# Kernel tuning notes

Hardware: AMD Instinct MI355X
Metric: run time of the kernel (lower is better)

Reference implementation:

```python
import jax, jax.numpy as jnp
import numpy as np

B, T, S, D, H, E, K, FF = 4, 1024, 1024, 1024, 16, 8, 2, 4096
DH = D // H
EPS = 1e-5

def layernorm(x, g, b):
    m = x.mean(-1, keepdims=True)
    v = x.var(-1, keepdims=True)
    return (x - m) / jnp.sqrt(v + EPS) * g + b

def mha(q, k, v, mask, wq, bq, wk, bk, wv, bv, wo, bo):
    Bq, Tq, _ = q.shape
    Tk = k.shape[1]
    Q = (q @ wq + bq).reshape(Bq, Tq, H, DH).transpose(0, 2, 1, 3)
    Kh = (k @ wk + bk).reshape(Bq, Tk, H, DH).transpose(0, 2, 1, 3)
    V = (v @ wv + bv).reshape(Bq, Tk, H, DH).transpose(0, 2, 1, 3)
    scores = jnp.einsum('bhqd,bhkd->bhqk', Q, Kh) / (DH ** 0.5)
    scores = jnp.where(mask != 0, scores, jnp.float32(-1e9))
    A = jax.nn.softmax(scores, axis=-1)
    O = jnp.einsum('bhqk,bhkd->bhqd', A, V).transpose(0, 2, 1, 3).reshape(Bq, Tq, D)
    return O @ wo + bo

def sparse_moe(x, wg, bg, w1, b1, w2, b2):
    # x: [B,T,D] -> tokens [N,D]
    Bx, Tx, _ = x.shape
    xt = x.reshape(-1, D)
    N = xt.shape[0]
    probs = jax.nn.softmax(xt @ wg + bg, axis=-1)          # [N,E]
    topv, topi = jax.lax.top_k(probs, K)                    # [N,K]
    topv = topv / topv.sum(-1, keepdims=True)
    gates = jnp.zeros((N, E), xt.dtype).at[jnp.arange(N)[:, None], topi].set(topv)
    h = jax.nn.relu(jnp.einsum('nd,edh->enh', xt, w1) + b1[:, None, :])  # [E,N,FF]
    y = jnp.einsum('enh,ehd->end', h, w2) + b2[:, None, :]               # [E,N,D]
    out = jnp.einsum('ne,end->nd', gates, y)
    return out.reshape(Bx, Tx, D)

def setup_inputs() -> dict:
    key = jax.random.key(0)
    ks = jax.random.split(key, 32)
    r = lambda k, s: jax.random.normal(k, s, dtype=jnp.float32) * 0.02
    inp = {
        'x': jax.random.normal(ks[0], (B, T, D), jnp.float32),
        'encoder_out': jax.random.normal(ks[1], (B, S, D), jnp.float32),
        'src_attn_mask': jnp.ones((B, 1, 1, S), jnp.int32),
        'tgt_attn_mask': jnp.tril(jnp.ones((T, T), jnp.int32))[None, None],
        'ln1_g': jnp.ones((D,), jnp.float32), 'ln1_b': jnp.zeros((D,), jnp.float32),
        'ln2_g': jnp.ones((D,), jnp.float32), 'ln2_b': jnp.zeros((D,), jnp.float32),
        'ln3_g': jnp.ones((D,), jnp.float32), 'ln3_b': jnp.zeros((D,), jnp.float32),
        'wq1': r(ks[2], (D, D)), 'bq1': jnp.zeros((D,), jnp.float32),
        'wk1': r(ks[3], (D, D)), 'bk1': jnp.zeros((D,), jnp.float32),
        'wv1': r(ks[4], (D, D)), 'bv1': jnp.zeros((D,), jnp.float32),
        'wo1': r(ks[5], (D, D)), 'bo1': jnp.zeros((D,), jnp.float32),
        'wq2': r(ks[6], (D, D)), 'bq2': jnp.zeros((D,), jnp.float32),
        'wk2': r(ks[7], (D, D)), 'bk2': jnp.zeros((D,), jnp.float32),
        'wv2': r(ks[8], (D, D)), 'bv2': jnp.zeros((D,), jnp.float32),
        'wo2': r(ks[9], (D, D)), 'bo2': jnp.zeros((D,), jnp.float32),
        'wg': r(ks[10], (D, E)), 'bg': jnp.zeros((E,), jnp.float32),
        'w1': r(ks[11], (E, D, FF)), 'b1': jnp.zeros((E, FF), jnp.float32),
        'w2': r(ks[12], (E, FF, D)), 'b2': jnp.zeros((E, D), jnp.float32),
    }
    return inp

def reference(x, encoder_out, src_attn_mask, tgt_attn_mask,
              ln1_g, ln1_b, ln2_g, ln2_b, ln3_g, ln3_b,
              wq1, bq1, wk1, bk1, wv1, bv1, wo1, bo1,
              wq2, bq2, wk2, bk2, wv2, bv2, wo2, bo2,
              wg, bg, w1, b1, w2, b2):
    # pre-norm residual: x + sublayer(LN(x)); dropout=0 (eval)
    n1 = layernorm(x, ln1_g, ln1_b)
    h1 = x + mha(n1, n1, n1, tgt_attn_mask, wq1, bq1, wk1, bk1, wv1, bv1, wo1, bo1)
    n2 = layernorm(h1, ln2_g, ln2_b)
    h2 = h1 + mha(n2, encoder_out, encoder_out, src_attn_mask, wq2, bq2, wk2, bk2, wv2, bv2, wo2, bo2)
    n3 = layernorm(h2, ln3_g, ln3_b)
    h3 = h2 + sparse_moe(n3, wg, bg, w1, b1, w2, b2)
    return h3
```

## Files before the change

### kernel.cpp

```cpp
#include <hip/hip_runtime.h>

typedef unsigned short u16;
typedef float f32x4 __attribute__((ext_vector_type(4)));
typedef short s16x8 __attribute__((ext_vector_type(8)));
typedef u16   u16x4 __attribute__((ext_vector_type(4)));

#define DEV static __device__ __forceinline__

DEV u16 f2b(float f){
  unsigned u = __builtin_bit_cast(unsigned, f);
  u += 0x7fffu + ((u >> 16) & 1u);
  return (u16)(u >> 16);
}
DEV float b2f(u16 h){ unsigned u = ((unsigned)h) << 16; return __builtin_bit_cast(float, u); }
DEV void tsplit(float v, u16& hv, u16& lv){
  unsigned u = __builtin_bit_cast(unsigned, v);
  hv = (u16)(u >> 16);
  float rest = v - __builtin_bit_cast(float, u & 0xffff0000u);
  lv = (u16)(__builtin_bit_cast(unsigned, rest) >> 16);
}
DEV float fexp2(float x){ float r; asm("v_exp_f32 %0, %1" : "=v"(r) : "v"(x)); return r; }

DEV void glds16(const u16* g, u16* l){
  __builtin_amdgcn_global_load_lds(
      (const __attribute__((address_space(1))) void*)g,
      (__attribute__((address_space(3))) void*)l, 16, 0, 0);
}

DEV f32x4 mfma3(s16x8 ah, s16x8 al, s16x8 bh, s16x8 bl, f32x4 c){
  c = __builtin_amdgcn_mfma_f32_16x16x32_bf16(ah, bh, c, 0, 0, 0);
  c = __builtin_amdgcn_mfma_f32_16x16x32_bf16(ah, bl, c, 0, 0, 0);
  c = __builtin_amdgcn_mfma_f32_16x16x32_bf16(al, bh, c, 0, 0, 0);
  return c;
}

constexpr int TT = 1024, DM = 1024, NE = 8, FFD = 4096;
constexpr int NTOK = 4096;

struct Ptr8 { const float* p[8]; };

__global__ __launch_bounds__(256) void trans8_k(Ptr8 srcs, u16* __restrict__ dh, u16* __restrict__ dl){
  __shared__ float tl[64][65];
  const float* src = srcs.p[blockIdx.z];
  u16* dsth = dh + (size_t)blockIdx.z * 1024 * 1024;
  u16* dstl = dl + (size_t)blockIdx.z * 1024 * 1024;
  const int tid = threadIdx.x;
  const int r0 = blockIdx.y * 64, c0 = blockIdx.x * 64;
  const int ty = tid >> 4, tx = tid & 15;
#pragma unroll
  for (int i = 0; i < 4; i++){
    int row = ty + i * 16;
    f32x4 v = *(const f32x4*)&src[(size_t)(r0 + row) * 1024 + c0 + tx * 4];
#pragma unroll
    for (int j = 0; j < 4; j++) tl[row][tx * 4 + j] = v[j];
  }
  __syncthreads();
#pragma unroll
  for (int i = 0; i < 4; i++){
    int drow = ty + i * 16;
    u16x4 oh, ol;
#pragma unroll
    for (int j = 0; j < 4; j++){
      float v = tl[tx * 4 + j][drow];
      u16 hh, ll; tsplit(v, hh, ll);
      oh[j] = hh; ol[j] = ll;
    }
    *(u16x4*)&dsth[(size_t)(c0 + drow) * 1024 + r0 + tx * 4] = oh;
    *(u16x4*)&dstl[(size_t)(c0 + drow) * 1024 + r0 + tx * 4] = ol;
  }
}

__global__ __launch_bounds__(256) void transb_k(const float* __restrict__ src0, u16* __restrict__ dst0, int R, int C){
  __shared__ float tl[64][65];
  const float* src = src0 + (size_t)blockIdx.z * R * C;
  u16* dst = dst0 + (size_t)blockIdx.z * R * C;
  const int tid = threadIdx.x;
  const int r0 = blockIdx.y * 64, c0 = blockIdx.x * 64;
  const int ty = tid >> 4, tx = tid & 15;
#pragma unroll
  for (int i = 0; i < 4; i++){
    int row = ty + i * 16;
    f32x4 v = *(const f32x4*)&src[(size_t)(r0 + row) * C + c0 + tx * 4];
#pragma unroll
    for (int j = 0; j < 4; j++) tl[row][tx * 4 + j] = v[j];
  }
  __syncthreads();
#pragma unroll
  for (int i = 0; i < 4; i++){
    int drow = ty + i * 16;
    u16x4 o;
#pragma unroll
    for (int j = 0; j < 4; j++) o[j] = f2b(tl[tx * 4 + j][drow]);
    *(u16x4*)&dst[(size_t)(c0 + drow) * R + r0 + tx * 4] = o;
  }
}

__global__ __launch_bounds__(256) void split_k(const float* __restrict__ src,
                                               u16* __restrict__ dh, u16* __restrict__ dl, int n4){
  int i = blockIdx.x * 256 + threadIdx.x;
  if (i < n4){
    f32x4 v = *(const f32x4*)&src[(size_t)i * 4];
    u16x4 oh, ol;
#pragma unroll
    for (int j = 0; j < 4; j++){ u16 hh, ll; tsplit(v[j], hh, ll); oh[j] = hh; ol[j] = ll; }
    *(u16x4*)&dh[(size_t)i * 4] = oh;
    *(u16x4*)&dl[(size_t)i * 4] = ol;
  }
}

__global__ __launch_bounds__(256) void ln_k(const float* __restrict__ x, const float* __restrict__ g,
                                            const float* __restrict__ b,
                                            u16* __restrict__ outH, u16* __restrict__ outL){
  __shared__ float red[8];
  const int row = blockIdx.x, tid = threadIdx.x, l = tid & 63, wave = tid >> 6;
  f32x4 v = *(const f32x4*)&x[(size_t)row * DM + tid * 4];
  float s = v[0] + v[1] + v[2] + v[3];
  float sq = v[0]*v[0] + v[1]*v[1] + v[2]*v[2] + v[3]*v[3];
#pragma unroll
  for (int m = 1; m < 64; m <<= 1){ s += __shfl_xor(s, m); sq += __shfl_xor(sq, m); }
  if (l == 0){ red[wave] = s; red[4 + wave] = sq; }
  __syncthreads();
  float tot = red[0] + red[1] + red[2] + red[3];
  float totq = red[4] + red[5] + red[6] + red[7];
  float mean = tot * (1.0f / DM);
  float var = totq * (1.0f / DM) - mean * mean;
  float rstd = rsqrtf(var + 1e-5f);
  f32x4 gg = *(const f32x4*)&g[tid * 4];
  f32x4 bb = *(const f32x4*)&b[tid * 4];
  u16x4 oh, ol;
#pragma unroll
  for (int j = 0; j < 4; j++){
    float y = (v[j] - mean) * rstd * gg[j] + bb[j];
    u16 hh, ll; tsplit(y, hh, ll); oh[j] = hh; ol[j] = ll;
  }
  *(u16x4*)&outH[(size_t)row * DM + tid * 4] = oh;
  if (outL) *(u16x4*)&outL[(size_t)row * DM + tid * 4] = ol;
}

struct QKVArgs {
  const u16* ah[3]; const u16* al[3]; const float* bias[3];
};

__global__ __launch_bounds__(256) void gemm_qkv3_k(
    QKVArgs args, const u16* __restrict__ Bhp, const u16* __restrict__ Blp,
    u16* __restrict__ QH, u16* __restrict__ QL,
    u16* __restrict__ KH, u16* __restrict__ KL,
    u16* __restrict__ VTH, u16* __restrict__ VTL)
{
  constexpr int K = DM;
  __shared__ alignas(16) u16 LAh[128 * 32], LAl[128 * 32];
  __shared__ alignas(16) u16 LBh[128 * 32], LBl[128 * 32];
  const int tid = threadIdx.x, l = tid & 63, wave = tid >> 6;
  const int seg = blockIdx.z;
  const int m0 = blockIdx.y * 128, n0 = blockIdx.x * 128;
  const int r0 = tid >> 2, seg8 = (tid & 3) * 8;
  const u16* gAh = args.ah[seg] + (size_t)(m0 + r0) * K + seg8;
  const u16* gAl = args.al[seg] + (size_t)(m0 + r0) * K + seg8;
  const u16* gBh = Bhp + (size_t)(seg * 1024 + n0 + r0) * K + seg8;
  const u16* gBl = Blp + (size_t)(seg * 1024 + n0 + r0) * K + seg8;
  u16* wAh = &LAh[wave * 512]; u16* wAl = &LAl[wave * 512];
  u16* wBh = &LBh[wave * 512]; u16* wBl = &LBl[wave * 512];
  const size_t K64 = (size_t)64 * K;
  f32x4 acc[4][4];
#pragma unroll
  for (int i = 0; i < 4; i++)
#pragma unroll
    for (int j = 0; j < 4; j++) acc[i][j] = f32x4{0.f, 0.f, 0.f, 0.f};
  const int wm = (wave >> 1) * 64, wn = (wave & 1) * 64;
  for (int kt = 0; kt < K; kt += 32){
    __syncthreads();
    glds16(gAh + kt, wAh); glds16(gAh + kt + K64, wAh + 2048);
    glds16(gAl + kt, wAl); glds16(gAl + kt + K64, wAl + 2048);
    glds16(gBh + kt, wBh); glds16(gBh + kt + K64, wBh + 2048);
    glds16(gBl + kt, wBl); glds16(gBl + kt + K64, wBl + 2048);
    __syncthreads();
    s16x8 afh[4], afl[4], bfh[4], bfl[4];
#pragma unroll
    for (int i = 0; i < 4; i++){
      int ar = (wm + i * 16 + (l & 15)) * 32 + (l >> 4) * 8;
      int br = (wn + i * 16 + (l & 15)) * 32 + (l >> 4) * 8;
      afh[i] = *(const s16x8*)&LAh[ar];
      afl[i] = *(const s16x8*)&LAl[ar];
      bfh[i] = *(const s16x8*)&LBh[br];
      bfl[i] = *(const s16x8*)&LBl[br];
    }
#pragma unroll
    for (int i = 0; i < 4; i++)
#pragma unroll
      for (int j = 0; j < 4; j++)
        acc[i][j] = mfma3(afh[i], afl[i], bfh[j], bfl[j], acc[i][j]);
  }
  const float* bp = args.bias[seg];
  u16* DH = (seg == 0) ? QH : KH;
  u16* DL = (seg == 0) ? QL : KL;
#pragma unroll
  for (int i = 0; i < 4; i++)
#pragma unroll
    for (int r = 0; r < 4; r++){
      int row = m0 + wm + i * 16 + (l >> 4) * 4 + r;
#pragma unroll
      for (int j = 0; j < 4; j++){
        int col = n0 + wn + j * 16 + (l & 15);
        float v = acc[i][j][r] + bp[col];
        u16 hv, lv; tsplit(v, hv, lv);
        if (seg == 2){
          int bb = row >> 10, tq = row & 1023, hh = col >> 6, dd = col & 63;
          size_t vi = ((size_t)((bb << 4) + hh) * 64 + dd) * 1024 + tq;
          VTH[vi] = hv; VTL[vi] = lv;
        } else {
          size_t idx = (size_t)row * 1024 + col;
          DH[idx] = hv; DL[idx] = lv;
        }
      }
    }
}

__global__ __launch_bounds__(256) void gemm_o64_k(
    const u16* __restrict__ Ahp, const u16* __restrict__ Alp,
    const u16* __restrict__ Bhp, const u16* __restrict__ Blp,
    const float* __restrict__ bias, const float* __restrict__ res,
    float* __restrict__ Cf)
{
  constexpr int K = DM;
  __shared__ alignas(16) u16 LAh[64 * 32], LAl[64 * 32];
  __shared__ alignas(16) u16 LBh[128 * 32], LBl[128 * 32];
  const int tid = threadIdx.x, l = tid & 63, wave = tid >> 6;
  const int m0 = blockIdx.y * 64, n0 = blockIdx.x * 128;
  const int rA = tid >> 2, seg8 = (tid & 3) * 8;
  const u16* gAh = Ahp + (size_t)(m0 + rA) * K + seg8;
  const u16* gAl = Alp + (size_t)(m0 + rA) * K + seg8;
  const u16* gBh = Bhp + (size_t)(n0 + rA) * K + seg8;
  const u16* gBl = Blp + (size_t)(n0 + rA) * K + seg8;
  u16* wAh = &LAh[wave * 512]; u16* wAl = &LAl[wave * 512];
  u16* wBh = &LBh[wave * 512]; u16* wBl = &LBl[wave * 512];
  const size_t K64 = (size_t)64 * K;
  f32x4 acc[2][4];
#pragma unroll
  for (int i = 0; i < 2; i++)
#pragma unroll
    for (int j = 0; j < 4; j++) acc[i][j] = f32x4{0.f, 0.f, 0.f, 0.f};
  const int wm = (wave >> 1) * 32, wn = (wave & 1) * 64;
  for (int kt = 0; kt < K; kt += 32){
    __syncthreads();
    glds16(gAh + kt, wAh);
    glds16(gAl + kt, wAl);
    glds16(gBh + kt, wBh); glds16(gBh + kt + K64, wBh + 2048);
    glds16(gBl + kt, wBl); glds16(gBl + kt + K64, wBl + 2048);
    __syncthreads();
    s16x8 afh[2], afl[2], bfh[4], bfl[4];
#pragma unroll
    for (int i = 0; i < 2; i++){
      int ar = (wm + i * 16 + (l & 15)) * 32 + (l >> 4) * 8;
      afh[i] = *(const s16x8*)&LAh[ar];
      afl[i] = *(const s16x8*)&LAl[ar];
    }
#pragma unroll
    for (int j = 0; j < 4; j++){
      int br = (wn + j * 16 + (l & 15)) * 32 + (l >> 4) * 8;
      bfh[j] = *(const s16x8*)&LBh[br];
      bfl[j] = *(const s16x8*)&LBl[br];
    }
#pragma unroll
    for (int i = 0; i < 2; i++)
#pragma unroll
      for (int j = 0; j < 4; j++)
        acc[i][j] = mfma3(afh[i], afl[i], bfh[j], bfl[j], acc[i][j]);
  }
#pragma unroll
  for (int i = 0; i < 2; i++)
#pragma unroll
    for (int r = 0; r < 4; r++){
      int row = m0 + wm + i * 16 + (l >> 4) * 4 + r;
#pragma unroll
      for (int j = 0; j < 4; j++){
        int col = n0 + wn + j * 16 + (l & 15);
        size_t idx = (size_t)row * 1024 + col;
        Cf[idx] = acc[i][j][r] + bias[col] + res[idx];
      }
    }
}

template<bool CAUSAL>
__global__ __launch_bounds__(512) void attn5_k(
    const u16* __restrict__ Qh, const u16* __restrict__ Ql,
    const u16* __restrict__ Kh, const u16* __restrict__ Kl,
    const u16* __restrict__ Vth, const u16* __restrict__ Vtl,
    const int* __restrict__ mask,
    float* __restrict__ OP0, float* __restrict__ OP1,
    float* __restrict__ LS0, float* __restrict__ LS1,
    int Tq, int Tk)
{
  constexpr float CS = 0.125f * 1.4426950408889634f;
  __shared__ alignas(16) u16 KhiL[2048], KloL[2048];
  __shared__ alignas(16) u16 VhiL[2048], VloL[2048];
  __shared__ alignas(16) u16 Plh[8][640], Pll[8][640];
  const int tid = threadIdx.x, l = tid & 63, wave = tid >> 6;
  const int id = blockIdx.x;
  const int bh = ((id >> 3) & 7) * 8 + (id & 7);
  const int b = bh >> 4, h = bh & 15;
  const int qt = (id >> 6) & 7, ks = id >> 9;
  const int q0 = qt * 128;
  float* __restrict__ OP = ks ? OP1 : OP0;
  float* __restrict__ LS = ks ? LS1 : LS0;
  const int ktBeg = ks * 512;
  int lim = CAUSAL ? (q0 + 128) : Tk;
  if (lim > Tk) lim = Tk;
  int ktEnd = (ks + 1) * 512;
  if (ktEnd > lim) ktEnd = lim;

  const int qr = q0 + wave * 16 + (l & 15);
  s16x8 qah[2], qal[2];
#pragma unroll
  for (int kb = 0; kb < 2; kb++){
    size_t base = (size_t)(b * Tq + qr) * DM + h * 64 + kb * 32 + (l >> 4) * 8;
    qah[kb] = *(const s16x8*)(Qh + base);
    qal[kb] = *(const s16x8*)(Ql + base);
  }

  const int sHalf = wave >> 2;
  const int sw = wave & 3;
  const int iS = sw * 64 + l;
  const int keyS = iS >> 3, cKS = iS & 7;
  const u16* gK = (sHalf ? Kl : Kh)
      + (size_t)(b * Tk + ktBeg + keyS) * DM + h * 64 + ((cKS ^ (keyS & 7)) * 8);
  u16* dK = (sHalf ? KloL : KhiL) + sw * 512;
  const int dS = iS >> 2, cVS = iS & 3;
  const size_t vgbase = (size_t)bh * 64 * 1024;
  const u16* gV = (sHalf ? Vtl : Vth)
      + vgbase + (size_t)dS * 1024 + ktBeg + ((cVS ^ ((dS >> 1) & 3)) * 8);
  u16* dV = (sHalf ? VloL : VhiL) + sw * 512;

  float lsum[4] = {0.f, 0.f, 0.f, 0.f};
  f32x4 oacc[4];
#pragma unroll
  for (int nb = 0; nb < 4; nb++) oacc[nb] = f32x4{0.f, 0.f, 0.f, 0.f};
  const int qgr = q0 + wave * 16 + (l >> 4) * 4;

  for (int kt = ktBeg; kt < ktEnd; kt += 32){
    __syncthreads();
    glds16(gK, dK); gK += (size_t)32 * DM;
    glds16(gV, dV); gV += 32;
    __syncthreads();

    f32x4 s[2];
#pragma unroll
    for (int n = 0; n < 2; n++){
      s[n] = f32x4{0.f, 0.f, 0.f, 0.f};
      const int key = n * 16 + (l & 15);
      const int sK = (key & 7);
#pragma unroll
      for (int kb = 0; kb < 2; kb++){
        const int cK = kb * 4 + (l >> 4);
        const int off = key * 64 + ((cK ^ sK) * 8);
        s16x8 kh = *(const s16x8*)&KhiL[off];
        s16x8 klo = *(const s16x8*)&KloL[off];
        s[n] = __builtin_amdgcn_mfma_f32_16x16x32_bf16(qah[kb], kh, s[n], 0, 0, 0);
        s[n] = __builtin_amdgcn_mfma_f32_16x16x32_bf16(qah[kb], klo, s[n], 0, 0, 0);
        s[n] = __builtin_amdgcn_mfma_f32_16x16x32_bf16(qal[kb], kh, s[n], 0, 0, 0);
      }
    }
    int key0 = kt + (l & 15), key1 = key0 + 16;
    int mv0 = 1, mv1 = 1;
    if (!CAUSAL && mask){ mv0 = mask[b * Tk + key0]; mv1 = mask[b * Tk + key1]; }
#pragma unroll
    for (int r = 0; r < 4; r++){
      float p0, p1;
      if (CAUSAL){
        int qg = qgr + r;
        p0 = (key0 <= qg) ? fexp2(s[0][r] * CS) : 0.f;
        p1 = (key1 <= qg) ? fexp2(s[1][r] * CS) : 0.f;
      } else {
        p0 = mv0 ? fexp2(s[0][r] * CS) : 0.f;
        p1 = mv1 ? fexp2(s[1][r] * CS) : 0.f;
      }
      lsum[r] += p0 + p1;
      int po = ((l >> 4) * 4 + r) * 40 + (l & 15);
      u16 h0, l0, h1, l1;
      tsplit(p0, h0, l0); tsplit(p1, h1, l1);
      Plh[wave][po] = h0;      Pll[wave][po] = l0;
      Plh[wave][po + 16] = h1; Pll[wave][po + 16] = l1;
    }
    s16x8 pah = *(const s16x8*)&Plh[wave][(l & 15) * 40 + (l >> 4) * 8];
    s16x8 pal = *(const s16x8*)&Pll[wave][(l & 15) * 40 + (l >> 4) * 8];
#pragma unroll
    for (int nb = 0; nb < 4; nb++){
      const int d = nb * 16 + (l & 15);
      const int off = d * 32 + (((l >> 4) ^ ((d >> 1) & 3)) * 8);
      s16x8 vfh = *(const s16x8*)&VhiL[off];
      s16x8 vfl = *(const s16x8*)&VloL[off];
      oacc[nb] = mfma3(pah, pal, vfh, vfl, oacc[nb]);
    }
  }
#pragma unroll
  for (int r = 0; r < 4; r++){
    float s = lsum[r];
    s += __shfl_xor(s, 1); s += __shfl_xor(s, 2);
    s += __shfl_xor(s, 4); s += __shfl_xor(s, 8);
    int qg = qgr + r;
    if ((l & 15) == 0) LS[(size_t)bh * 1024 + qg] = s;
#pragma unroll
    for (int nb = 0; nb < 4; nb++)
      OP[(size_t)(b * Tq + qg) * DM + h * 64 + nb * 16 + (l & 15)] = oacc[nb][r];
  }
}

__global__ __launch_bounds__(256) void norm_k(
    const float* __restrict__ OP0, const float* __restrict__ OP1,
    const float* __restrict__ LS0, const float* __restrict__ LS1,
    u16* __restrict__ Oh, u16* __restrict__ Ol)
{
  const int t = blockIdx.x, c = threadIdx.x * 4;
  const int b = t >> 10, q = t & 1023, h = c >> 6;
  const size_t li = (size_t)(b * 16 + h) * 1024 + q;
  float inv = 1.0f / (LS0[li] + LS1[li]);
  f32x4 o0 = *(const f32x4*)&OP0[(size_t)t * DM + c];
  f32x4 o1 = *(const f32x4*)&OP1[(size_t)t * DM + c];
  u16x4 oh, ol;
#pragma unroll
  for (int j = 0; j < 4; j++){
    float v = (o0[j] + o1[j]) * inv;
    u16 hh, ll; tsplit(v, hh, ll); oh[j] = hh; ol[j] = ll;
  }
  *(u16x4*)&Oh[(size_t)t * DM + c] = oh;
  *(u16x4*)&Ol[(size_t)t * DM + c] = ol;
}

__global__ __launch_bounds__(256) void moe_gate_k(const float* __restrict__ X,
    const float* __restrict__ g3, const float* __restrict__ b3,
    const float* __restrict__ wg, const float* __restrict__ bg,
    int* __restrict__ cnt, int* __restrict__ perm,
    int* __restrict__ toke, int* __restrict__ tokp, float* __restrict__ tokg)
{
  const int wave = threadIdx.x >> 6, l = threadIdx.x & 63;
  const int t = blockIdx.x * 4 + wave;
  float xv[16];
  float s = 0.f, sq = 0.f;
#pragma unroll
  for (int i = 0; i < 16; i++){
    xv[i] = X[(size_t)t * DM + l + i * 64];
    s += xv[i]; sq += xv[i] * xv[i];
  }
#pragma unroll
  for (int m = 1; m < 64; m <<= 1){ s += __shfl_xor(s, m); sq += __shfl_xor(sq, m); }
  float mean = s * (1.0f / DM);
  float var = sq * (1.0f / DM) - mean * mean;
  float rstd = rsqrtf(var + 1e-5f);
  float acc[8];
#pragma unroll
  for (int e = 0; e < 8; e++) acc[e] = 0.f;
#pragma unroll
  for (int i = 0; i < 16; i++){
    int k = l + i * 64;
    float xn = (xv[i] - mean) * rstd * g3[k] + b3[k];
    f32x4 wa = *(const f32x4*)&wg[k * 8];
    f32x4 wb = *(const f32x4*)&wg[k * 8 + 4];
#pragma unroll
    for (int j = 0; j < 4; j++){ acc[j] += xn * wa[j]; acc[4 + j] += xn * wb[j]; }
  }
#pragma unroll
  for (int e = 0; e < 8; e++)
#pragma unroll
    for (int m = 1; m < 64; m <<= 1) acc[e] += __shfl_xor(acc[e], m);
  if (l == 0){
    float lg[8];
#pragma unroll
    for (int e = 0; e < 8; e++) lg[e] = acc[e] + bg[e];
    float mx = lg[0];
#pragma unroll
    for (int e = 1; e < 8; e++) mx = fmaxf(mx, lg[e]);
    float ex[8]; float sum = 0.f;
#pragma unroll
    for (int e = 0; e < 8; e++){ ex[e] = expf(lg[e] - mx); sum += ex[e]; }
    int i0 = 0;
    for (int e = 1; e < 8; e++) if (ex[e] > ex[i0]) i0 = e;
    int i1 = (i0 == 0) ? 1 : 0;
    for (int e = 0; e < 8; e++) if (e != i0 && ex[e] > ex[i1]) i1 = e;
    float p0 = ex[i0] / sum, p1 = ex[i1] / sum;
    float gs = p0 + p1;
    int pos0 = atomicAdd(&cnt[i0], 1);
    int pos1 = atomicAdd(&cnt[i1], 1);
    perm[i0 * 4096 + pos0] = t;
    perm[i1 * 4096 + pos1] = t;
    toke[2 * t] = i0; toke[2 * t + 1] = i1;
    tokp[2 * t] = pos0; tokp[2 * t + 1] = pos1;
    tokg[2 * t] = p0 / gs; tokg[2 * t + 1] = p1 / gs;
  }
}

__global__ void offsets_k(const int* __restrict__ cnt, int* __restrict__ off){
  if (threadIdx.x == 0){
    int a = 0;
    for (int e = 0; e < 8; e++){ off[e] = a; a += cnt[e]; }
  }
}

__global__ __launch_bounds__(256) void gemm_moe1_k(
    const u16* __restrict__ X, const u16* __restrict__ W1t, const float* __restrict__ b1,
    const int* __restrict__ perm, const int* __restrict__ cnt, const int* __restrict__ off,
    u16* __restrict__ Hb)
{
  const int e = blockIdx.z;
  const int Ce = cnt[e];
  const int mt = blockIdx.y;
  if (mt * 128 >= Ce) return;
  __shared__ alignas(16) u16 Asl[128 * 32];
  __shared__ alignas(16) u16 Bsl[128 * 32];
  const int tid = threadIdx.x, l = tid & 63, wave = tid >> 6;
  const int n0 = blockIdx.x * 128;
  const int r0 = tid >> 2, seg = (tid & 3) * 8;
  const int rl0 = mt * 128 + r0, rl1 = rl0 + 64;
  const int g0 = perm[e * 4096 + (rl0 < Ce ? rl0 : Ce - 1)];
  const int g1 = perm[e * 4096 + (rl1 < Ce ? rl1 : Ce - 1)];
  const u16* gA0 = X + (size_t)g0 * DM + seg;
  const u16* gA1 = X + (size_t)g1 * DM + seg;
  const u16* gB = W1t + (size_t)e * FFD * DM + (size_t)(n0 + r0) * DM + seg;
  u16* wA = &Asl[wave * 512]; u16* wB = &Bsl[wave * 512];
  f32x4 acc[4][4];
#pragma unroll
  for (int i = 0; i < 4; i++)
#pragma unroll
    for (int j = 0; j < 4; j++) acc[i][j] = f32x4{0.f,0.f,0.f,0.f};
  const int wm = (wave >> 1) * 64, wn = (wave & 1) * 64;
  for (int kt = 0; kt < DM; kt += 32){
    __syncthreads();
    glds16(gA0 + kt, wA); glds16(gA1 + kt, wA + 2048);
    glds16(gB + kt, wB);  glds16(gB + kt + (size_t)64 * DM, wB + 2048);
    __syncthreads();
    s16x8 af[4], bfr[4];
#pragma unroll
    for (int i = 0; i < 4; i++){
      af[i]  = *(const s16x8*)&Asl[(wm + i * 16 + (l & 15)) * 32 + (l >> 4) * 8];
      bfr[i] = *(const s16x8*)&Bsl[(wn + i * 16 + (l & 15)) * 32 + (l >> 4) * 8];
    }
#pragma unroll
    for (int i = 0; i < 4; i++)
#pragma unroll
      for (int j = 0; j < 4; j++)
        acc[i][j] = __builtin_amdgcn_mfma_f32_16x16x32_bf16(af[i], bfr[j], acc[i][j], 0, 0, 0);
  }
  const int base = off[e];
#pragma unroll
  for (int i = 0; i < 4; i++)
#pragma unroll
    for (int r = 0; r < 4; r++){
      int rloc = mt * 128 + wm + i * 16 + (l >> 4) * 4 + r;
      if (rloc < Ce){
#pragma unroll
        for (int j = 0; j < 4; j++){
          int col = n0 + wn + j * 16 + (l & 15);
          float v = acc[i][j][r] + b1[e * FFD + col];
          v = fmaxf(v, 0.f);
          Hb[(size_t)(base + rloc) * FFD + col] = f2b(v);
        }
      }
    }
}

__global__ __launch_bounds__(256) void gemm_moe2_k(
    const u16* __restrict__ Hb, const u16* __restrict__ W2t,
    const int* __restrict__ cnt, const int* __restrict__ off, float* __restrict__ Y)
{
  const int e = blockIdx.z;
  const int Ce = cnt[e];
  const int mt = blockIdx.y;
  if (mt * 128 >= Ce) return;
  __shared__ alignas(16) u16 Asl[128 * 32];
  __shared__ alignas(16) u16 Bsl[128 * 32];
  const int tid = threadIdx.x, l = tid & 63, wave = tid >> 6;
  const int n0 = blockIdx.x * 128;
  const int r0 = tid >> 2, seg = (tid & 3) * 8;
  const int base = off[e];
  const int rl0 = mt * 128 + r0, rl1 = rl0 + 64;
  const int a0r = base + (rl0 < Ce ? rl0 : Ce - 1);
  const int a1r = base + (rl1 < Ce ? rl1 : Ce - 1);
  const u16* gA0 = Hb + (size_t)a0r * FFD + seg;
  const u16* gA1 = Hb + (size_t)a1r * FFD + seg;
  const u16* gB = W2t + (size_t)e * DM * FFD + (size_t)(n0 + r0) * FFD + seg;
  u16* wA = &Asl[wave * 512]; u16* wB = &Bsl[wave * 512];
  f32x4 acc[4][4];
#pragma unroll
  for (int i = 0; i < 4; i++)
#pragma unroll
    for (int j = 0; j < 4; j++) acc[i][j] = f32x4{0.f,0.f,0.f,0.f};
  const int wm = (wave >> 1) * 64, wn = (wave & 1) * 64;
  for (int kt = 0; kt < FFD; kt += 32){
    __syncthreads();
    glds16(gA0 + kt, wA); glds16(gA1 + kt, wA + 2048);
    glds16(gB + kt, wB);  glds16(gB + kt + (size_t)64 * FFD, wB + 2048);
    __syncthreads();
    s16x8 af[4], bfr[4];
#pragma unroll
    for (int i = 0; i < 4; i++){
      af[i]  = *(const s16x8*)&Asl[(wm + i * 16 + (l & 15)) * 32 + (l >> 4) * 8];
      bfr[i] = *(const s16x8*)&Bsl[(wn + i * 16 + (l & 15)) * 32 + (l >> 4) * 8];
    }
#pragma unroll
    for (int i = 0; i < 4; i++)
#pragma unroll
      for (int j = 0; j < 4; j++)
        acc[i][j] = __builtin_amdgcn_mfma_f32_16x16x32_bf16(af[i], bfr[j], acc[i][j], 0, 0, 0);
  }
#pragma unroll
  for (int i = 0; i < 4; i++)
#pragma unroll
    for (int r = 0; r < 4; r++){
      int rloc = mt * 128 + wm + i * 16 + (l >> 4) * 4 + r;
      if (rloc < Ce){
#pragma unroll
        for (int j = 0; j < 4; j++){
          int col = n0 + wn + j * 16 + (l & 15);
          Y[(size_t)(base + rloc) * DM + col] = acc[i][j][r];
        }
      }
    }
}

__global__ __launch_bounds__(256) void combine_k(const float* __restrict__ h2, const float* __restrict__ Y,
    const int* __restrict__ toke, const int* __restrict__ tokp, const float* __restrict__ tokg,
    const int* __restrict__ off, const float* __restrict__ b2, float* __restrict__ out)
{
  const int t = blockIdx.x;
  const int c = threadIdx.x * 4;
  int e0 = toke[2 * t], e1 = toke[2 * t + 1];
  size_t r0 = (size_t)off[e0] + tokp[2 * t];
  size_t r1 = (size_t)off[e1] + tokp[2 * t + 1];
  float g0 = tokg[2 * t], g1 = tokg[2 * t + 1];
  f32x4 a  = *(const f32x4*)&h2[(size_t)t * DM + c];
  f32x4 y0 = *(const f32x4*)&Y[r0 * DM + c];
  f32x4 y1 = *(const f32x4*)&Y[r1 * DM + c];
  f32x4 v0 = *(const f32x4*)&b2[(size_t)e0 * DM + c];
  f32x4 v1 = *(const f32x4*)&b2[(size_t)e1 * DM + c];
  f32x4 o = a + (y0 + v0) * g0 + (y1 + v1) * g1;
  *(f32x4*)&out[(size_t)t * DM + c] = o;
}

extern "C" void kernel_launch(void* const* d_in, const int* in_sizes, int n_in,
                              void* d_out, int out_size, void* d_ws, size_t ws_size,
                              hipStream_t stream) {
  const float* x    = (const float*)d_in[0];
  const float* enc  = (const float*)d_in[1];
  const int* smask  = (const int*)d_in[2];
  const float* ln1g = (const float*)d_in[4]; const float* ln1b = (const float*)d_in[5];
  const float* ln2g = (const float*)d_in[6]; const float* ln2b = (const float*)d_in[7];
  const float* ln3g = (const float*)d_in[8]; const float* ln3b = (const float*)d_in[9];
  const float* wq1 = (const float*)d_in[10]; const float* bq1 = (const float*)d_in[11];
  const float* wk1 = (const float*)d_in[12]; const float* bk1 = (const float*)d_in[13];
  const float* wv1 = (const float*)d_in[14]; const float* bv1 = (const float*)d_in[15];
  const float* wo1 = (const float*)d_in[16]; const float* bo1 = (const float*)d_in[17];
  const float* wq2 = (const float*)d_in[18]; const float* bq2 = (const float*)d_in[19];
  const float* wk2 = (const float*)d_in[20]; const float* bk2 = (const float*)d_in[21];
  const float* wv2 = (const float*)d_in[22]; const float* bv2 = (const float*)d_in[23];
  const float* wo2 = (const float*)d_in[24]; const float* bo2 = (const float*)d_in[25];
  const float* wg  = (const float*)d_in[26]; const float* bg  = (const float*)d_in[27];
  const float* w1  = (const float*)d_in[28]; const float* b1  = (const float*)d_in[29];
  const float* w2  = (const float*)d_in[30]; const float* b2  = (const float*)d_in[31];

  const size_t MB = 1024ull * 1024ull;
  char* ws = (char*)d_ws;
  size_t o = 0;
  auto alloc = [&](size_t bytes) -> void* {
    void* p = ws + o;
    o += (bytes + 255) & ~(size_t)255;
    return p;
  };
  float* H1  = (float*)alloc(16 * MB);
  float* H2  = (float*)alloc(16 * MB);
  u16*  NBF  = (u16*) alloc(8 * MB);
  int* CNT  = (int*)alloc(256);
  int* OFF  = (int*)alloc(256);
  int* PERM = (int*)alloc((size_t)8 * 4096 * 4);
  int* TOKE = (int*)alloc((size_t)NTOK * 2 * 4);
  int* TOKP = (int*)alloc((size_t)NTOK * 2 * 4);
  float* TOKG = (float*)alloc((size_t)NTOK * 2 * 4);
  char* R = (char*)alloc(224 * MB);
  u16* WTH = (u16*)(R);
  u16* WTL = (u16*)(R + 16 * MB);
  u16* NH  = (u16*)(R + 32 * MB);
  u16* NL  = (u16*)(R + 40 * MB);
  u16* EH  = (u16*)(R + 48 * MB);
  u16* EL  = (u16*)(R + 56 * MB);
  u16* QH  = (u16*)(R + 64 * MB);
  u16* QL  = (u16*)(R + 72 * MB);
  u16* KH  = (u16*)(R + 80 * MB);
  u16* KL  = (u16*)(R + 88 * MB);
  u16* VTH = (u16*)(R + 96 * MB);
  u16* VTL = (u16*)(R + 104 * MB);
  u16* OH  = (u16*)(R + 112 * MB);
  u16* OL  = (u16*)(R + 120 * MB);
  float* OP0 = (float*)(R + 128 * MB);
  float* OP1 = (float*)(R + 144 * MB);
  float* LS0 = (float*)(R + 160 * MB);
  float* LS1 = (float*)(R + 161 * MB);
  u16* W1T = (u16*)(R);
  u16* W2T = (u16*)(R + 64 * MB);
  u16* HB  = (u16*)(R + 128 * MB);
  float* YB = (float*)(R + 192 * MB);

  Ptr8 p8; p8.p[0]=wq1; p8.p[1]=wk1; p8.p[2]=wv1; p8.p[3]=wo1;
           p8.p[4]=wq2; p8.p[5]=wk2; p8.p[6]=wv2; p8.p[7]=wo2;
  trans8_k<<<dim3(16,16,8), 256, 0, stream>>>(p8, WTH, WTL);
  split_k<<<dim3(4096), 256, 0, stream>>>(enc, EH, EL, NTOK * DM / 4);

  const size_t W = (size_t)1024 * 1024;
  ln_k<<<dim3(NTOK), 256, 0, stream>>>(x, ln1g, ln1b, NH, NL);
  {
    QKVArgs a;
    a.ah[0]=NH; a.ah[1]=NH; a.ah[2]=NH;
    a.al[0]=NL; a.al[1]=NL; a.al[2]=NL;
    a.bias[0]=bq1; a.bias[1]=bk1; a.bias[2]=bv1;
    gemm_qkv3_k<<<dim3(8,32,3), 256, 0, stream>>>(a, WTH + 0*W, WTL + 0*W,
                                                  QH, QL, KH, KL, VTH, VTL);
  }
  attn5_k<true><<<dim3(1024), 512, 0, stream>>>(QH, QL, KH, KL, VTH, VTL, nullptr,
                                                OP0, OP1, LS0, LS1, TT, TT);
  norm_k<<<dim3(NTOK), 256, 0, stream>>>(OP0, OP1, LS0, LS1, OH, OL);
  gemm_o64_k<<<dim3(8,64), 256, 0, stream>>>(OH, OL, WTH + 3*W, WTL + 3*W, bo1, x, H1);

  ln_k<<<dim3(NTOK), 256, 0, stream>>>(H1, ln2g, ln2b, NH, NL);
  {
    QKVArgs a;
    a.ah[0]=NH; a.ah[1]=EH; a.ah[2]=EH;
    a.al[0]=NL; a.al[1]=EL; a.al[2]=EL;
    a.bias[0]=bq2; a.bias[1]=bk2; a.bias[2]=bv2;
    gemm_qkv3_k<<<dim3(8,32,3), 256, 0, stream>>>(a, WTH + 4*W, WTL + 4*W,
                                                  QH, QL, KH, KL, VTH, VTL);
  }
  attn5_k<false><<<dim3(1024), 512, 0, stream>>>(QH, QL, KH, KL, VTH, VTL, smask,
                                                 OP0, OP1, LS0, LS1, TT, TT);
  norm_k<<<dim3(NTOK), 256, 0, stream>>>(OP0, OP1, LS0, LS1, OH, OL);
  gemm_o64_k<<<dim3(8,64), 256, 0, stream>>>(OH, OL, WTH + 7*W, WTL + 7*W, bo2, H1, H2);

  transb_k<<<dim3(64,16,8), 256, 0, stream>>>(w1, W1T, 1024, 4096);
  transb_k<<<dim3(16,64,8), 256, 0, stream>>>(w2, W2T, 4096, 1024);
  ln_k<<<dim3(NTOK), 256, 0, stream>>>(H2, ln3g, ln3b, NBF, nullptr);
  hipMemsetAsync(CNT, 0, 8 * sizeof(int), stream);
  moe_gate_k<<<dim3(1024), 256, 0, stream>>>(H2, ln3g, ln3b, wg, bg, CNT, PERM, TOKE, TOKP, TOKG);
  offsets_k<<<dim3(1), 64, 0, stream>>>(CNT, OFF);
  gemm_moe1_k<<<dim3(32,32,8), 256, 0, stream>>>(NBF, W1T, b1, PERM, CNT, OFF, HB);
  gemm_moe2_k<<<dim3(8,32,8), 256, 0, stream>>>(HB, W2T, CNT, OFF, YB);
  combine_k<<<dim3(NTOK), 256, 0, stream>>>(H2, YB, TOKE, TOKP, TOKG, OFF, b2, (float*)d_out);
}
```

Before: 955.8 us.

## Use K=64 stages in MoE GEMMs, split-K the second MoE GEMM with bf16 partials

Both MoE GEMMs now load two 32-wide K slices per barrier pair, which halves the number of __syncthreads per K and doubles LDS use. The second MoE GEMM splits K into two halves across a doubled grid z dimension to raise block count. It writes bf16 partial outputs that combine_k sums, cutting write traffic but adding bf16 rounding on each partial.

```diff
diff --git a/kernel.cpp b/kernel.cpp
--- a/kernel.cpp
+++ b/kernel.cpp
@@ -503,8 +503,8 @@
   const int Ce = cnt[e];
   const int mt = blockIdx.y;
   if (mt * 128 >= Ce) return;
-  __shared__ alignas(16) u16 Asl[128 * 32];
-  __shared__ alignas(16) u16 Bsl[128 * 32];
+  __shared__ alignas(16) u16 Asl[2][128 * 32];
+  __shared__ alignas(16) u16 Bsl[2][128 * 32];
   const int tid = threadIdx.x, l = tid & 63, wave = tid >> 6;
   const int n0 = blockIdx.x * 128;
   const int r0 = tid >> 2, seg = (tid & 3) * 8;
@@ -514,29 +514,36 @@
   const u16* gA0 = X + (size_t)g0 * DM + seg;
   const u16* gA1 = X + (size_t)g1 * DM + seg;
   const u16* gB = W1t + (size_t)e * FFD * DM + (size_t)(n0 + r0) * DM + seg;
-  u16* wA = &Asl[wave * 512]; u16* wB = &Bsl[wave * 512];
+  const size_t B64 = (size_t)64 * DM;
+  u16* wA0 = &Asl[0][wave * 512]; u16* wA1 = &Asl[1][wave * 512];
+  u16* wB0 = &Bsl[0][wave * 512]; u16* wB1 = &Bsl[1][wave * 512];
   f32x4 acc[4][4];
 #pragma unroll
   for (int i = 0; i < 4; i++)
 #pragma unroll
     for (int j = 0; j < 4; j++) acc[i][j] = f32x4{0.f,0.f,0.f,0.f};
   const int wm = (wave >> 1) * 64, wn = (wave & 1) * 64;
-  for (int kt = 0; kt < DM; kt += 32){
-    __syncthreads();
-    glds16(gA0 + kt, wA); glds16(gA1 + kt, wA + 2048);
-    glds16(gB + kt, wB);  glds16(gB + kt + (size_t)64 * DM, wB + 2048);
-    __syncthreads();
-    s16x8 af[4], bfr[4];
-#pragma unroll
-    for (int i = 0; i < 4; i++){
-      af[i]  = *(const s16x8*)&Asl[(wm + i * 16 + (l & 15)) * 32 + (l >> 4) * 8];
-      bfr[i] = *(const s16x8*)&Bsl[(wn + i * 16 + (l & 15)) * 32 + (l >> 4) * 8];
-    }
-#pragma unroll
-    for (int i = 0; i < 4; i++)
-#pragma unroll
-      for (int j = 0; j < 4; j++)
-        acc[i][j] = __builtin_amdgcn_mfma_f32_16x16x32_bf16(af[i], bfr[j], acc[i][j], 0, 0, 0);
+  for (int kt = 0; kt < DM; kt += 64){
+    __syncthreads();
+    glds16(gA0 + kt, wA0);      glds16(gA1 + kt, wA0 + 2048);
+    glds16(gA0 + kt + 32, wA1); glds16(gA1 + kt + 32, wA1 + 2048);
+    glds16(gB + kt, wB0);       glds16(gB + kt + B64, wB0 + 2048);
+    glds16(gB + kt + 32, wB1);  glds16(gB + kt + 32 + B64, wB1 + 2048);
+    __syncthreads();
+#pragma unroll
+    for (int p = 0; p < 2; p++){
+      s16x8 af[4], bfr[4];
+#pragma unroll
+      for (int i = 0; i < 4; i++){
+        af[i]  = *(const s16x8*)&Asl[p][(wm + i * 16 + (l & 15)) * 32 + (l >> 4) * 8];
+        bfr[i] = *(const s16x8*)&Bsl[p][(wn + i * 16 + (l & 15)) * 32 + (l >> 4) * 8];
+      }
+#pragma unroll
+      for (int i = 0; i < 4; i++)
+#pragma unroll
+        for (int j = 0; j < 4; j++)
+          acc[i][j] = __builtin_amdgcn_mfma_f32_16x16x32_bf16(af[i], bfr[j], acc[i][j], 0, 0, 0);
+    }
   }
   const int base = off[e];
 #pragma unroll
@@ -558,14 +565,17 @@
 
 __global__ __launch_bounds__(256) void gemm_moe2_k(
     const u16* __restrict__ Hb, const u16* __restrict__ W2t,
-    const int* __restrict__ cnt, const int* __restrict__ off, float* __restrict__ Y)
+    const int* __restrict__ cnt, const int* __restrict__ off,
+    u16* __restrict__ YP0, u16* __restrict__ YP1)
 {
-  const int e = blockIdx.z;
+  const int z = blockIdx.z;
+  const int e = z & 7, ks = z >> 3;
   const int Ce = cnt[e];
   const int mt = blockIdx.y;
   if (mt * 128 >= Ce) return;
-  __shared__ alignas(16) u16 Asl[128 * 32];
-  __shared__ alignas(16) u16 Bsl[128 * 32];
+  u16* __restrict__ Y = ks ? YP1 : YP0;
+  __shared__ alignas(16) u16 Asl[2][128 * 32];
+  __shared__ alignas(16) u16 Bsl[2][128 * 32];
   const int tid = threadIdx.x, l = tid & 63, wave = tid >> 6;
   const int n0 = blockIdx.x * 128;
   const int r0 = tid >> 2, seg = (tid & 3) * 8;
@@ -576,29 +586,37 @@
   const u16* gA0 = Hb + (size_t)a0r * FFD + seg;
   const u16* gA1 = Hb + (size_t)a1r * FFD + seg;
   const u16* gB = W2t + (size_t)e * DM * FFD + (size_t)(n0 + r0) * FFD + seg;
-  u16* wA = &Asl[wave * 512]; u16* wB = &Bsl[wave * 512];
+  const size_t B64 = (size_t)64 * FFD;
+  u16* wA0 = &Asl[0][wave * 512]; u16* wA1 = &Asl[1][wave * 512];
+  u16* wB0 = &Bsl[0][wave * 512]; u16* wB1 = &Bsl[1][wave * 512];
   f32x4 acc[4][4];
 #pragma unroll
   for (int i = 0; i < 4; i++)
 #pragma unroll
     for (int j = 0; j < 4; j++) acc[i][j] = f32x4{0.f,0.f,0.f,0.f};
   const int wm = (wave >> 1) * 64, wn = (wave & 1) * 64;
-  for (int kt = 0; kt < FFD; kt += 32){
-    __syncthreads();
-    glds16(gA0 + kt, wA); glds16(gA1 + kt, wA + 2048);
-    glds16(gB + kt, wB);  glds16(gB + kt + (size_t)64 * FFD, wB + 2048);
-    __syncthreads();
-    s16x8 af[4], bfr[4];
-#pragma unroll
-    for (int i = 0; i < 4; i++){
-      af[i]  = *(const s16x8*)&Asl[(wm + i * 16 + (l & 15)) * 32 + (l >> 4) * 8];
-      bfr[i] = *(const s16x8*)&Bsl[(wn + i * 16 + (l & 15)) * 32 + (l >> 4) * 8];
-    }
-#pragma unroll
-    for (int i = 0; i < 4; i++)
-#pragma unroll
-      for (int j = 0; j < 4; j++)
-        acc[i][j] = __builtin_amdgcn_mfma_f32_16x16x32_bf16(af[i], bfr[j], acc[i][j], 0, 0, 0);
+  const int kBeg = ks * (FFD / 2), kEnd = kBeg + FFD / 2;
+  for (int kt = kBeg; kt < kEnd; kt += 64){
+    __syncthreads();
+    glds16(gA0 + kt, wA0);      glds16(gA1 + kt, wA0 + 2048);
+    glds16(gA0 + kt + 32, wA1); glds16(gA1 + kt + 32, wA1 + 2048);
+    glds16(gB + kt, wB0);       glds16(gB + kt + B64, wB0 + 2048);
+    glds16(gB + kt + 32, wB1);  glds16(gB + kt + 32 + B64, wB1 + 2048);
+    __syncthreads();
+#pragma unroll
+    for (int p = 0; p < 2; p++){
+      s16x8 af[4], bfr[4];
+#pragma unroll
+      for (int i = 0; i < 4; i++){
+        af[i]  = *(const s16x8*)&Asl[p][(wm + i * 16 + (l & 15)) * 32 + (l >> 4) * 8];
+        bfr[i] = *(const s16x8*)&Bsl[p][(wn + i * 16 + (l & 15)) * 32 + (l >> 4) * 8];
+      }
+#pragma unroll
+      for (int i = 0; i < 4; i++)
+#pragma unroll
+        for (int j = 0; j < 4; j++)
+          acc[i][j] = __builtin_amdgcn_mfma_f32_16x16x32_bf16(af[i], bfr[j], acc[i][j], 0, 0, 0);
+    }
   }
 #pragma unroll
   for (int i = 0; i < 4; i++)
@@ -609,13 +627,14 @@
 #pragma unroll
         for (int j = 0; j < 4; j++){
           int col = n0 + wn + j * 16 + (l & 15);
-          Y[(size_t)(base + rloc) * DM + col] = acc[i][j][r];
+          Y[(size_t)(base + rloc) * DM + col] = f2b(acc[i][j][r]);
         }
       }
     }
 }
 
-__global__ __launch_bounds__(256) void combine_k(const float* __restrict__ h2, const float* __restrict__ Y,
+__global__ __launch_bounds__(256) void combine_k(const float* __restrict__ h2,
+    const u16* __restrict__ YP0, const u16* __restrict__ YP1,
     const int* __restrict__ toke, const int* __restrict__ tokp, const float* __restrict__ tokg,
     const int* __restrict__ off, const float* __restrict__ b2, float* __restrict__ out)
 {
@@ -626,11 +645,19 @@
   size_t r1 = (size_t)off[e1] + tokp[2 * t + 1];
   float g0 = tokg[2 * t], g1 = tokg[2 * t + 1];
   f32x4 a  = *(const f32x4*)&h2[(size_t)t * DM + c];
-  f32x4 y0 = *(const f32x4*)&Y[r0 * DM + c];
-  f32x4 y1 = *(const f32x4*)&Y[r1 * DM + c];
+  u16x4 ya0 = *(const u16x4*)&YP0[r0 * DM + c];
+  u16x4 ya1 = *(const u16x4*)&YP1[r0 * DM + c];
+  u16x4 yb0 = *(const u16x4*)&YP0[r1 * DM + c];
+  u16x4 yb1 = *(const u16x4*)&YP1[r1 * DM + c];
   f32x4 v0 = *(const f32x4*)&b2[(size_t)e0 * DM + c];
   f32x4 v1 = *(const f32x4*)&b2[(size_t)e1 * DM + c];
-  f32x4 o = a + (y0 + v0) * g0 + (y1 + v1) * g1;
+  f32x4 o;
+#pragma unroll
+  for (int j = 0; j < 4; j++){
+    float yA = b2f(ya0[j]) + b2f(ya1[j]);
+    float yB = b2f(yb0[j]) + b2f(yb1[j]);
+    o[j] = a[j] + (yA + v0[j]) * g0 + (yB + v1[j]) * g1;
+  }
   *(f32x4*)&out[(size_t)t * DM + c] = o;
 }
 
@@ -694,7 +721,8 @@
   u16* W1T = (u16*)(R);
   u16* W2T = (u16*)(R + 64 * MB);
   u16* HB  = (u16*)(R + 128 * MB);
-  float* YB = (float*)(R + 192 * MB);
+  u16* YP0 = (u16*)(R + 192 * MB);
+  u16* YP1 = (u16*)(R + 208 * MB);
 
   Ptr8 p8; p8.p[0]=wq1; p8.p[1]=wk1; p8.p[2]=wv1; p8.p[3]=wo1;
            p8.p[4]=wq2; p8.p[5]=wk2; p8.p[6]=wv2; p8.p[7]=wo2;
@@ -737,6 +765,6 @@
   moe_gate_k<<<dim3(1024), 256, 0, stream>>>(H2, ln3g, ln3b, wg, bg, CNT, PERM, TOKE, TOKP, TOKG);
   offsets_k<<<dim3(1), 64, 0, stream>>>(CNT, OFF);
   gemm_moe1_k<<<dim3(32,32,8), 256, 0, stream>>>(NBF, W1T, b1, PERM, CNT, OFF, HB);
-  gemm_moe2_k<<<dim3(8,32,8), 256, 0, stream>>>(HB, W2T, CNT, OFF, YB);
-  combine_k<<<dim3(NTOK), 256, 0, stream>>>(H2, YB, TOKE, TOKP, TOKG, OFF, b2, (float*)d_out);
-}
+  gemm_moe2_k<<<dim3(8,32,16), 256, 0, stream>>>(HB, W2T, CNT, OFF, YP0, YP1);
+  combine_k<<<dim3(NTOK), 256, 0, stream>>>(H2, YP0, YP1, TOKE, TOKP, TOKG, OFF, b2, (float*)d_out);
+}
```

Measured after the change: 902.6 us. 5.6% less time.
